# Performance work log

Measured on AMD Instinct MI355X. Metric: run time of the kernel, lower is better.

The kernel has to match this reference:

```python
import jax, jax.numpy as jnp
import numpy as np

B, T, I = 16384, 50, 5
H = 128
PRED_LEN = 12


def _uniform(key, shape, bound):
    return jax.random.uniform(key, shape, jnp.float32, -bound, bound)


def setup_inputs() -> dict:
    key = jax.random.key(0)
    ks = jax.random.split(key, 12)
    bound = 1.0 / np.sqrt(H)  # PyTorch LSTM/Linear default init
    return {
        "x": jax.random.normal(ks[0], (B, T, I), jnp.float32),
        "enc_Wih": _uniform(ks[1], (4 * H, I), bound),
        "enc_Whh": _uniform(ks[2], (4 * H, H), bound),
        "enc_bih": _uniform(ks[3], (4 * H,), bound),
        "enc_bhh": _uniform(ks[4], (4 * H,), bound),
        "dec_Wih": _uniform(ks[5], (4 * H, I), bound),
        "dec_Whh": _uniform(ks[6], (4 * H, H), bound),
        "dec_bih": _uniform(ks[7], (4 * H,), bound),
        "dec_bhh": _uniform(ks[8], (4 * H,), bound),
        "lin_W": _uniform(ks[9], (2, H), bound),
        "lin_b": _uniform(ks[10], (2,), bound),
    }


def _lstm_cell(x_t, h, c, Wih, Whh, bih, bhh):
    # PyTorch gate order: i, f, g, o
    gates = x_t @ Wih.T + h @ Whh.T + (bih + bhh)  # [B, 4H]
    i, f, g, o = jnp.split(gates, 4, axis=-1)
    i = jax.nn.sigmoid(i)
    f = jax.nn.sigmoid(f)
    g = jnp.tanh(g)
    o = jax.nn.sigmoid(o)
    c_new = f * c + i * g
    h_new = o * jnp.tanh(c_new)
    return h_new, c_new


def reference(x, enc_Wih, enc_Whh, enc_bih, enc_bhh,
              dec_Wih, dec_Whh, dec_bih, dec_bhh, lin_W, lin_b):
    b = x.shape[0]
    h0 = jnp.zeros((b, H), x.dtype)
    c0 = jnp.zeros((b, H), x.dtype)

    # ---- encoder LSTM over the history sequence ----
    def enc_step(carry, x_t):
        h, c = carry
        h, c = _lstm_cell(x_t, h, c, enc_Wih, enc_Whh, enc_bih, enc_bhh)
        return (h, c), None

    (h, c), _ = jax.lax.scan(enc_step, (h0, c0), jnp.swapaxes(x, 0, 1))

    static_context = x[:, -1, 2:]          # [B, I-2]
    last_velocity = x[:, -1, :2]           # [B, 2]
    dec_in0 = jnp.concatenate([last_velocity, static_context], axis=1)  # [B, I]

    def dec_step(carry, _):
        h, c, dec_in = carry
        h, c = _lstm_cell(dec_in, h, c, dec_Wih, dec_Whh, dec_bih, dec_bhh)
        pred = h @ lin_W.T + lin_b                      # [B, 2]
        dec_in = jnp.concatenate([pred, static_context], axis=1)
        return (h, c, dec_in), pred

    _, preds = jax.lax.scan(dec_step, (h, c, dec_in0), None, length=PRED_LEN)
    return jnp.swapaxes(preds, 0, 1)  # [B, pred_len, 2]
```

## Files before the change

### kernel.cpp

```cpp
#include <hip/hip_runtime.h>
#include <cstdint>

#define TT 50
#define II 5
#define PRED 12
#define SAMP 32
#define NSB 2

typedef _Float16 f16;
typedef _Float16 f16x8 __attribute__((ext_vector_type(8)));
typedef float f32x4 __attribute__((ext_vector_type(4)));

__device__ __forceinline__ float fsig(float x) {
    return __builtin_amdgcn_rcpf(1.f + __builtin_amdgcn_exp2f(-1.4426950408889634f * x));
}
__device__ __forceinline__ float ftanh(float x) {
    return 1.f - 2.f * __builtin_amdgcn_rcpf(1.f + __builtin_amdgcn_exp2f(2.885390081777927f * x));
}

__device__ __forceinline__ void mfma(f32x4& d, f16x8 a, f16x8 b) {
    asm("v_mfma_f32_16x16x32_f16 %0, %1, %2, %0" : "+v"(d) : "v"(a), "v"(b));
}

__device__ __forceinline__ void load_frags(const float* __restrict__ Wih,
                                           const float* __restrict__ Whh,
                                           const float* __restrict__ bih,
                                           const float* __restrict__ bhh,
                                           int w, int q, int cl, f16x8 wr[4][5]) {
    #pragma unroll
    for (int gs = 0; gs < 4; ++gs) {
        const int gw = gs * 128 + w * 16 + cl;
        const float* whr = Whh + gw * 128 + q * 8;
        #pragma unroll
        for (int kc = 0; kc < 4; ++kc) {
            f32x4 a = *(const f32x4*)(whr + kc * 32);
            f32x4 b = *(const f32x4*)(whr + kc * 32 + 4);
            f16x8 f;
            f[0] = (f16)a[0]; f[1] = (f16)a[1]; f[2] = (f16)a[2]; f[3] = (f16)a[3];
            f[4] = (f16)b[0]; f[5] = (f16)b[1]; f[6] = (f16)b[2]; f[7] = (f16)b[3];
            wr[gs][kc] = f;
        }
        f16x8 f;
        #pragma unroll
        for (int j = 0; j < 8; ++j) f[j] = (f16)0.f;
        if (q == 0) {
            f[0] = (f16)Wih[gw * 5 + 0]; f[1] = (f16)Wih[gw * 5 + 1];
            f[2] = (f16)Wih[gw * 5 + 2]; f[3] = (f16)Wih[gw * 5 + 3];
            f[4] = (f16)Wih[gw * 5 + 4];
            f[5] = (f16)(bih[gw] + bhh[gw]);
        }
        wr[gs][4] = f;
    }
}

__global__ __launch_bounds__(512, 2)
void lstm_kernel(const float* __restrict__ x,
                 const float* __restrict__ eWih, const float* __restrict__ eWhh,
                 const float* __restrict__ ebih, const float* __restrict__ ebhh,
                 const float* __restrict__ dWih, const float* __restrict__ dWhh,
                 const float* __restrict__ dbih, const float* __restrict__ dbhh,
                 const float* __restrict__ linW, const float* __restrict__ linB,
                 float* __restrict__ out) {
    __shared__ __align__(16) unsigned char state[2 * SAMP * 256];
    __shared__ __align__(16) f16 xstage[52 * SAMP * 8];
    __shared__ float predpart[8][SAMP][2];

    const int tid  = threadIdx.x;
    const int lane = tid & 63;
    const int w    = tid >> 6;
    const int q    = lane >> 4;
    const int cl   = lane & 15;
    const int s0   = blockIdx.x * SAMP;
    const int jb   = w * 16 + q * 4;
    const int fswz = (2 * (cl & 7)) | (cl >> 3);

    int hro[4];
    #pragma unroll
    for (int kc = 0; kc < 4; ++kc)
        hro[kc] = cl * 256 + (((kc * 4 + q) ^ fswz) & 15) * 16;
    const int physh = ((jb >> 3) ^ fswz) & 15;
    const int hwo   = cl * 256 + physh * 16 + (jb & 7) * 2;

    {
        uint32_t* sp = (uint32_t*)state;
        #pragma unroll
        for (int r = 0; r < 4; ++r) sp[tid + r * 512] = 0u;
    }
    #pragma unroll
    for (int k = 0; k < 4; ++k) {
        int c = tid + k * 512;
        if (c < TT * SAMP) {
            int t = c >> 5, s = c & 31;
            const float* xr = x + (size_t)(s0 + s) * (TT * II) + t * II;
            union { f16 h[8]; uint4 u; } pk;
            pk.h[0] = (f16)xr[0]; pk.h[1] = (f16)xr[1]; pk.h[2] = (f16)xr[2];
            pk.h[3] = (f16)xr[3]; pk.h[4] = (f16)xr[4];
            pk.h[5] = (f16)1.f;  pk.h[6] = (f16)0.f;  pk.h[7] = (f16)0.f;
            *(uint4*)(xstage + (t * SAMP + s) * 8) = pk.u;
        }
    }

    f16x8 wr[4][5];
    load_frags(eWih, eWhh, ebih, ebhh, w, q, cl, wr);

    float creg[NSB][4];
    #pragma unroll
    for (int ns = 0; ns < NSB; ++ns)
        #pragma unroll
        for (int i = 0; i < 4; ++i) creg[ns][i] = 0.f;

    __syncthreads();

    #pragma unroll 1
    for (int t = 0; t < TT; ++t) {
        const int curoff = (t & 1) << 13;
        const int nxtoff = curoff ^ 8192;
        #pragma unroll
        for (int ns = 0; ns < NSB; ++ns) {
            const unsigned char* cb = state + curoff + ns * 4096;
            f16x8 bx = *(const f16x8*)(xstage + (t * SAMP + ns * 16 + cl) * 8);
            f16x8 b0 = *(const f16x8*)(cb + hro[0]);
            f32x4 a0 = {0.f, 0.f, 0.f, 0.f};
            f32x4 a1 = {0.f, 0.f, 0.f, 0.f};
            f32x4 a2 = {0.f, 0.f, 0.f, 0.f};
            f32x4 a3 = {0.f, 0.f, 0.f, 0.f};
            mfma(a0, wr[0][0], b0);
            mfma(a1, wr[1][0], b0);
            mfma(a2, wr[2][0], b0);
            mfma(a3, wr[3][0], b0);
            #pragma unroll
            for (int kc = 1; kc < 4; ++kc) {
                f16x8 bh = *(const f16x8*)(cb + hro[kc]);
                mfma(a0, wr[0][kc], bh);
                mfma(a1, wr[1][kc], bh);
                mfma(a2, wr[2][kc], bh);
                mfma(a3, wr[3][kc], bh);
            }
            mfma(a0, wr[0][4], bx);
            mfma(a1, wr[1][4], bx);
            mfma(a2, wr[2][4], bx);
            mfma(a3, wr[3][4], bx);

            union { f16 h[4]; uint2 u; } pk;
            #pragma unroll
            for (int idx = 0; idx < 4; ++idx) {
                float ii = fsig(a0[idx]);
                float ff = fsig(a1[idx]);
                float gg = ftanh(a2[idx]);
                float oo = fsig(a3[idx]);
                float cn = ff * creg[ns][idx] + ii * gg;
                creg[ns][idx] = cn;
                pk.h[idx] = (f16)(oo * ftanh(cn));
            }
            *(uint2*)(state + nxtoff + ns * 4096 + hwo) = pk.u;
        }
        __syncthreads();
    }

    load_frags(dWih, dWhh, dbih, dbhh, w, q, cl, wr);
    f16 w0h[4], w1h[4];
    #pragma unroll
    for (int idx = 0; idx < 4; ++idx) {
        w0h[idx] = (f16)linW[jb + idx];
        w1h[idx] = (f16)linW[128 + jb + idx];
    }
    float sc0 = 0.f, sc1 = 0.f, sc2 = 0.f, lb0 = 0.f, lb1 = 0.f;
    if (tid < SAMP) {
        const float* xr = x + (size_t)(s0 + tid) * (TT * II) + 49 * II;
        sc0 = xr[2]; sc1 = xr[3]; sc2 = xr[4];
        lb0 = linB[0]; lb1 = linB[1];
    }

    #pragma unroll 1
    for (int td = 0; td < PRED; ++td) {
        const int curoff = (td & 1) << 13;
        const int nxtoff = curoff ^ 8192;
        const int xslot  = (td == 0) ? 49 : (50 + (td & 1));
        float p0s[NSB], p1s[NSB];
        #pragma unroll
        for (int ns = 0; ns < NSB; ++ns) {
            const unsigned char* cb = state + curoff + ns * 4096;
            f16x8 bx = *(const f16x8*)(xstage + (xslot * SAMP + ns * 16 + cl) * 8);
            f16x8 b0 = *(const f16x8*)(cb + hro[0]);
            f32x4 a0 = {0.f, 0.f, 0.f, 0.f};
            f32x4 a1 = {0.f, 0.f, 0.f, 0.f};
            f32x4 a2 = {0.f, 0.f, 0.f, 0.f};
            f32x4 a3 = {0.f, 0.f, 0.f, 0.f};
            mfma(a0, wr[0][0], b0);
            mfma(a1, wr[1][0], b0);
            mfma(a2, wr[2][0], b0);
            mfma(a3, wr[3][0], b0);
            #pragma unroll
            for (int kc = 1; kc < 4; ++kc) {
                f16x8 bh = *(const f16x8*)(cb + hro[kc]);
                mfma(a0, wr[0][kc], bh);
                mfma(a1, wr[1][kc], bh);
                mfma(a2, wr[2][kc], bh);
                mfma(a3, wr[3][kc], bh);
            }
            mfma(a0, wr[0][4], bx);
            mfma(a1, wr[1][4], bx);
            mfma(a2, wr[2][4], bx);
            mfma(a3, wr[3][4], bx);

            float p0 = 0.f, p1 = 0.f;
            union { f16 h[4]; uint2 u; } pk;
            #pragma unroll
            for (int idx = 0; idx < 4; ++idx) {
                float ii = fsig(a0[idx]);
                float ff = fsig(a1[idx]);
                float gg = ftanh(a2[idx]);
                float oo = fsig(a3[idx]);
                float cn = ff * creg[ns][idx] + ii * gg;
                creg[ns][idx] = cn;
                float hv = oo * ftanh(cn);
                p0 += hv * (float)w0h[idx];
                p1 += hv * (float)w1h[idx];
                pk.h[idx] = (f16)hv;
            }
            *(uint2*)(state + nxtoff + ns * 4096 + hwo) = pk.u;
            p0 += __shfl_xor(p0, 16); p0 += __shfl_xor(p0, 32);
            p1 += __shfl_xor(p1, 16); p1 += __shfl_xor(p1, 32);
            p0s[ns] = p0; p1s[ns] = p1;
        }
        if (q == 0) {
            #pragma unroll
            for (int ns = 0; ns < NSB; ++ns) {
                predpart[w][ns * 16 + cl][0] = p0s[ns];
                predpart[w][ns * 16 + cl][1] = p1s[ns];
            }
        }
        __syncthreads();
        if (tid < SAMP) {
            float a0 = lb0, a1 = lb1;
            #pragma unroll
            for (int ww = 0; ww < 8; ++ww) {
                a0 += predpart[ww][tid][0];
                a1 += predpart[ww][tid][1];
            }
            float2 o2; o2.x = a0; o2.y = a1;
            *(float2*)(out + (size_t)(s0 + tid) * (PRED * 2) + td * 2) = o2;
            union { f16 h[8]; uint4 u; } pk;
            pk.h[0] = (f16)a0;  pk.h[1] = (f16)a1;
            pk.h[2] = (f16)sc0; pk.h[3] = (f16)sc1; pk.h[4] = (f16)sc2;
            pk.h[5] = (f16)1.f; pk.h[6] = (f16)0.f; pk.h[7] = (f16)0.f;
            int ws = 50 + ((td + 1) & 1);
            *(uint4*)(xstage + (ws * SAMP + tid) * 8) = pk.u;
        }
        __syncthreads();
    }
}

extern "C" void kernel_launch(void* const* d_in, const int* in_sizes, int n_in,
                              void* d_out, int out_size, void* d_ws, size_t ws_size,
                              hipStream_t stream) {
    (void)in_sizes; (void)n_in; (void)out_size; (void)d_ws; (void)ws_size;
    const float* x    = (const float*)d_in[0];
    const float* eWih = (const float*)d_in[1];
    const float* eWhh = (const float*)d_in[2];
    const float* ebih = (const float*)d_in[3];
    const float* ebhh = (const float*)d_in[4];
    const float* dWih = (const float*)d_in[5];
    const float* dWhh = (const float*)d_in[6];
    const float* dbih = (const float*)d_in[7];
    const float* dbhh = (const float*)d_in[8];
    const float* linW = (const float*)d_in[9];
    const float* linB = (const float*)d_in[10];

    lstm_kernel<<<512, 512, 0, stream>>>(x, eWih, eWhh, ebih, ebhh,
                                         dWih, dWhh, dbih, dbhh,
                                         linW, linB, (float*)d_out);
}
```

Baseline: 311.2 us.

## Ping-pong two sample groups per block to overlap MFMA with gate math

Each block now handles 64 samples split into two independent 32-sample groups, each with its own hidden-state buffer and cell registers. The encoder and decoder loops alternate between the groups, issuing one group's matrix multiplies while the other group runs its sigmoid/tanh gate math. The intent is to hide the dependency between each step's MFMAs and the VALU work that follows them. The cost is half as many blocks (256), more live accumulator registers, larger LDS use, and more barriers per step in the decoder.

Result: faster. 284.7 us (-8.5%).

```diff
diff --git a/kernel.cpp b/kernel.cpp
--- a/kernel.cpp
+++ b/kernel.cpp
@@ -4,8 +4,6 @@
 #define TT 50
 #define II 5
 #define PRED 12
-#define SAMP 32
-#define NSB 2
 
 typedef _Float16 f16;
 typedef _Float16 f16x8 __attribute__((ext_vector_type(8)));
@@ -16,10 +14,6 @@
 }
 __device__ __forceinline__ float ftanh(float x) {
     return 1.f - 2.f * __builtin_amdgcn_rcpf(1.f + __builtin_amdgcn_exp2f(2.885390081777927f * x));
-}
-
-__device__ __forceinline__ void mfma(f32x4& d, f16x8 a, f16x8 b) {
-    asm("v_mfma_f32_16x16x32_f16 %0, %1, %2, %0" : "+v"(d) : "v"(a), "v"(b));
 }
 
 __device__ __forceinline__ void load_frags(const float* __restrict__ Wih,
@@ -50,6 +44,102 @@
             f[5] = (f16)(bih[gw] + bhh[gw]);
         }
         wr[gs][4] = f;
+    }
+}
+
+__device__ __forceinline__ void mfma_group(f32x4 (&acc)[4][2],
+        const unsigned char* hb, const f16* xrow,
+        const f16x8 (&wr)[4][5],
+        const int (&hro)[4], int cl) {
+    const f32x4 z4 = {0.f, 0.f, 0.f, 0.f};
+    #pragma unroll
+    for (int ns = 0; ns < 2; ++ns) {
+        const unsigned char* cb = hb + ns * 4096;
+        f16x8 bx = *(const f16x8*)(xrow + (ns * 16 + cl) * 8);
+        f16x8 b0 = *(const f16x8*)(cb + hro[0]);
+        acc[0][ns] = __builtin_amdgcn_mfma_f32_16x16x32_f16(wr[0][0], b0, z4, 0, 0, 0);
+        acc[1][ns] = __builtin_amdgcn_mfma_f32_16x16x32_f16(wr[1][0], b0, z4, 0, 0, 0);
+        acc[2][ns] = __builtin_amdgcn_mfma_f32_16x16x32_f16(wr[2][0], b0, z4, 0, 0, 0);
+        acc[3][ns] = __builtin_amdgcn_mfma_f32_16x16x32_f16(wr[3][0], b0, z4, 0, 0, 0);
+        #pragma unroll
+        for (int kc = 1; kc < 4; ++kc) {
+            f16x8 bh = *(const f16x8*)(cb + hro[kc]);
+            acc[0][ns] = __builtin_amdgcn_mfma_f32_16x16x32_f16(wr[0][kc], bh, acc[0][ns], 0, 0, 0);
+            acc[1][ns] = __builtin_amdgcn_mfma_f32_16x16x32_f16(wr[1][kc], bh, acc[1][ns], 0, 0, 0);
+            acc[2][ns] = __builtin_amdgcn_mfma_f32_16x16x32_f16(wr[2][kc], bh, acc[2][ns], 0, 0, 0);
+            acc[3][ns] = __builtin_amdgcn_mfma_f32_16x16x32_f16(wr[3][kc], bh, acc[3][ns], 0, 0, 0);
+        }
+        acc[0][ns] = __builtin_amdgcn_mfma_f32_16x16x32_f16(wr[0][4], bx, acc[0][ns], 0, 0, 0);
+        acc[1][ns] = __builtin_amdgcn_mfma_f32_16x16x32_f16(wr[1][4], bx, acc[1][ns], 0, 0, 0);
+        acc[2][ns] = __builtin_amdgcn_mfma_f32_16x16x32_f16(wr[2][4], bx, acc[2][ns], 0, 0, 0);
+        acc[3][ns] = __builtin_amdgcn_mfma_f32_16x16x32_f16(wr[3][4], bx, acc[3][ns], 0, 0, 0);
+    }
+}
+
+__device__ __forceinline__ void valu_enc(f32x4 (&acc)[4][2], float (&cr)[2][4],
+        unsigned char* hb, int hwo) {
+    #pragma unroll
+    for (int ns = 0; ns < 2; ++ns) {
+        union { f16 h[4]; uint2 u; } pk;
+        #pragma unroll
+        for (int idx = 0; idx < 4; ++idx) {
+            float ii = fsig(acc[0][ns][idx]);
+            float ff = fsig(acc[1][ns][idx]);
+            float gg = ftanh(acc[2][ns][idx]);
+            float oo = fsig(acc[3][ns][idx]);
+            float cn = ff * cr[ns][idx] + ii * gg;
+            cr[ns][idx] = cn;
+            pk.h[idx] = (f16)(oo * ftanh(cn));
+        }
+        *(uint2*)(hb + ns * 4096 + hwo) = pk.u;
+    }
+}
+
+__device__ __forceinline__ void valu_dec(f32x4 (&acc)[4][2], float (&cr)[2][4],
+        unsigned char* hb, int hwo,
+        const f16 (&w0h)[4], const f16 (&w1h)[4],
+        float (*pp)[32][2], int w, int q, int cl) {
+    #pragma unroll
+    for (int ns = 0; ns < 2; ++ns) {
+        union { f16 h[4]; uint2 u; } pk;
+        float p0 = 0.f, p1 = 0.f;
+        #pragma unroll
+        for (int idx = 0; idx < 4; ++idx) {
+            float ii = fsig(acc[0][ns][idx]);
+            float ff = fsig(acc[1][ns][idx]);
+            float gg = ftanh(acc[2][ns][idx]);
+            float oo = fsig(acc[3][ns][idx]);
+            float cn = ff * cr[ns][idx] + ii * gg;
+            cr[ns][idx] = cn;
+            float hv = oo * ftanh(cn);
+            p0 += hv * (float)w0h[idx];
+            p1 += hv * (float)w1h[idx];
+            pk.h[idx] = (f16)hv;
+        }
+        *(uint2*)(hb + ns * 4096 + hwo) = pk.u;
+        p0 += __shfl_xor(p0, 16); p0 += __shfl_xor(p0, 32);
+        p1 += __shfl_xor(p1, 16); p1 += __shfl_xor(p1, 32);
+        if (q == 0) { pp[w][ns * 16 + cl][0] = p0; pp[w][ns * 16 + cl][1] = p1; }
+    }
+}
+
+__device__ __forceinline__ void finalize(int g, int tdf, int tid, int s0,
+        const float (*pp)[32][2], float lb0, float lb1,
+        f16* xstage, float* __restrict__ out) {
+    if (tid < 32) {
+        float a0 = lb0, a1 = lb1;
+        #pragma unroll
+        for (int ww = 0; ww < 8; ++ww) { a0 += pp[ww][tid][0]; a1 += pp[ww][tid][1]; }
+        const int s = g * 32 + tid;
+        float2 o2; o2.x = a0; o2.y = a1;
+        *(float2*)(out + (size_t)(s0 + s) * (PRED * 2) + tdf * 2) = o2;
+        if (tdf < PRED - 1) {
+            uint4 row = *(const uint4*)(xstage + (49 * 64 + s) * 8);
+            union { f16 h[2]; uint32_t u; } pk2;
+            pk2.h[0] = (f16)a0; pk2.h[1] = (f16)a1;
+            row.x = pk2.u;
+            *(uint4*)(xstage + ((50 + g) * 64 + s) * 8) = row;
+        }
     }
 }
 
@@ -61,16 +151,16 @@
                  const float* __restrict__ dbih, const float* __restrict__ dbhh,
                  const float* __restrict__ linW, const float* __restrict__ linB,
                  float* __restrict__ out) {
-    __shared__ __align__(16) unsigned char state[2 * SAMP * 256];
-    __shared__ __align__(16) f16 xstage[52 * SAMP * 8];
-    __shared__ float predpart[8][SAMP][2];
+    __shared__ __align__(16) unsigned char hstate[2 * 8192];
+    __shared__ __align__(16) f16 xstage[52 * 64 * 8];
+    __shared__ float predpart[2][8][32][2];
 
     const int tid  = threadIdx.x;
     const int lane = tid & 63;
     const int w    = tid >> 6;
     const int q    = lane >> 4;
     const int cl   = lane & 15;
-    const int s0   = blockIdx.x * SAMP;
+    const int s0   = blockIdx.x * 64;
     const int jb   = w * 16 + q * 4;
     const int fswz = (2 * (cl & 7)) | (cl >> 3);
 
@@ -82,80 +172,55 @@
     const int hwo   = cl * 256 + physh * 16 + (jb & 7) * 2;
 
     {
-        uint32_t* sp = (uint32_t*)state;
-        #pragma unroll
-        for (int r = 0; r < 4; ++r) sp[tid + r * 512] = 0u;
-    }
-    #pragma unroll
-    for (int k = 0; k < 4; ++k) {
+        uint32_t* sp = (uint32_t*)hstate;
+        #pragma unroll
+        for (int r = 0; r < 8; ++r) sp[tid + r * 512] = 0u;
+    }
+    #pragma unroll
+    for (int k = 0; k < 7; ++k) {
         int c = tid + k * 512;
-        if (c < TT * SAMP) {
-            int t = c >> 5, s = c & 31;
+        if (c < TT * 64) {
+            int t = c >> 6, s = c & 63;
             const float* xr = x + (size_t)(s0 + s) * (TT * II) + t * II;
             union { f16 h[8]; uint4 u; } pk;
             pk.h[0] = (f16)xr[0]; pk.h[1] = (f16)xr[1]; pk.h[2] = (f16)xr[2];
             pk.h[3] = (f16)xr[3]; pk.h[4] = (f16)xr[4];
             pk.h[5] = (f16)1.f;  pk.h[6] = (f16)0.f;  pk.h[7] = (f16)0.f;
-            *(uint4*)(xstage + (t * SAMP + s) * 8) = pk.u;
+            *(uint4*)(xstage + (t * 64 + s) * 8) = pk.u;
         }
     }
 
     f16x8 wr[4][5];
     load_frags(eWih, eWhh, ebih, ebhh, w, q, cl, wr);
 
-    float creg[NSB][4];
-    #pragma unroll
-    for (int ns = 0; ns < NSB; ++ns)
-        #pragma unroll
-        for (int i = 0; i < 4; ++i) creg[ns][i] = 0.f;
-
-    __syncthreads();
-
+    float creg0[2][4], creg1[2][4];
+    #pragma unroll
+    for (int ns = 0; ns < 2; ++ns)
+        #pragma unroll
+        for (int i = 0; i < 4; ++i) { creg0[ns][i] = 0.f; creg1[ns][i] = 0.f; }
+
+    f32x4 accA[4][2], accB[4][2];
+    unsigned char* hb0 = hstate;
+    unsigned char* hb1 = hstate + 8192;
+
+    __syncthreads();
+
+    mfma_group(accA, hb0, xstage + 0, wr, hro, cl);
+    __syncthreads();
     #pragma unroll 1
-    for (int t = 0; t < TT; ++t) {
-        const int curoff = (t & 1) << 13;
-        const int nxtoff = curoff ^ 8192;
-        #pragma unroll
-        for (int ns = 0; ns < NSB; ++ns) {
-            const unsigned char* cb = state + curoff + ns * 4096;
-            f16x8 bx = *(const f16x8*)(xstage + (t * SAMP + ns * 16 + cl) * 8);
-            f16x8 b0 = *(const f16x8*)(cb + hro[0]);
-            f32x4 a0 = {0.f, 0.f, 0.f, 0.f};
-            f32x4 a1 = {0.f, 0.f, 0.f, 0.f};
-            f32x4 a2 = {0.f, 0.f, 0.f, 0.f};
-            f32x4 a3 = {0.f, 0.f, 0.f, 0.f};
-            mfma(a0, wr[0][0], b0);
-            mfma(a1, wr[1][0], b0);
-            mfma(a2, wr[2][0], b0);
-            mfma(a3, wr[3][0], b0);
-            #pragma unroll
-            for (int kc = 1; kc < 4; ++kc) {
-                f16x8 bh = *(const f16x8*)(cb + hro[kc]);
-                mfma(a0, wr[0][kc], bh);
-                mfma(a1, wr[1][kc], bh);
-                mfma(a2, wr[2][kc], bh);
-                mfma(a3, wr[3][kc], bh);
-            }
-            mfma(a0, wr[0][4], bx);
-            mfma(a1, wr[1][4], bx);
-            mfma(a2, wr[2][4], bx);
-            mfma(a3, wr[3][4], bx);
-
-            union { f16 h[4]; uint2 u; } pk;
-            #pragma unroll
-            for (int idx = 0; idx < 4; ++idx) {
-                float ii = fsig(a0[idx]);
-                float ff = fsig(a1[idx]);
-                float gg = ftanh(a2[idx]);
-                float oo = fsig(a3[idx]);
-                float cn = ff * creg[ns][idx] + ii * gg;
-                creg[ns][idx] = cn;
-                pk.h[idx] = (f16)(oo * ftanh(cn));
-            }
-            *(uint2*)(state + nxtoff + ns * 4096 + hwo) = pk.u;
-        }
-        __syncthreads();
-    }
+    for (int j = 0; j < 49; ++j) {
+        valu_enc(accA, creg0, hb0, hwo);
+        mfma_group(accB, hb1, xstage + (j * 64 + 32) * 8, wr, hro, cl);
+        __syncthreads();
+        valu_enc(accB, creg1, hb1, hwo);
+        mfma_group(accA, hb0, xstage + ((j + 1) * 64) * 8, wr, hro, cl);
+        __syncthreads();
+    }
+    valu_enc(accA, creg0, hb0, hwo);
+    mfma_group(accB, hb1, xstage + (49 * 64 + 32) * 8, wr, hro, cl);
+    __syncthreads();
+    valu_enc(accB, creg1, hb1, hwo);
+    __syncthreads();
 
     load_frags(dWih, dWhh, dbih, dbhh, w, q, cl, wr);
     f16 w0h[4], w1h[4];
@@ -164,91 +229,31 @@
         w0h[idx] = (f16)linW[jb + idx];
         w1h[idx] = (f16)linW[128 + jb + idx];
     }
-    float sc0 = 0.f, sc1 = 0.f, sc2 = 0.f, lb0 = 0.f, lb1 = 0.f;
-    if (tid < SAMP) {
-        const float* xr = x + (size_t)(s0 + tid) * (TT * II) + 49 * II;
-        sc0 = xr[2]; sc1 = xr[3]; sc2 = xr[4];
-        lb0 = linB[0]; lb1 = linB[1];
-    }
-
+    const float lb0 = linB[0], lb1 = linB[1];
+
+    mfma_group(accA, hb0, xstage + (49 * 64) * 8, wr, hro, cl);
+    __syncthreads();
+    valu_dec(accA, creg0, hb0, hwo, w0h, w1h, predpart[0], w, q, cl);
+    mfma_group(accB, hb1, xstage + (49 * 64 + 32) * 8, wr, hro, cl);
+    __syncthreads();
     #pragma unroll 1
-    for (int td = 0; td < PRED; ++td) {
-        const int curoff = (td & 1) << 13;
-        const int nxtoff = curoff ^ 8192;
-        const int xslot  = (td == 0) ? 49 : (50 + (td & 1));
-        float p0s[NSB], p1s[NSB];
-        #pragma unroll
-        for (int ns = 0; ns < NSB; ++ns) {
-            const unsigned char* cb = state + curoff + ns * 4096;
-            f16x8 bx = *(const f16x8*)(xstage + (xslot * SAMP + ns * 16 + cl) * 8);
-            f16x8 b0 = *(const f16x8*)(cb + hro[0]);
-            f32x4 a0 = {0.f, 0.f, 0.f, 0.f};
-            f32x4 a1 = {0.f, 0.f, 0.f, 0.f};
-            f32x4 a2 = {0.f, 0.f, 0.f, 0.f};
-            f32x4 a3 = {0.f, 0.f, 0.f, 0.f};
-            mfma(a0, wr[0][0], b0);
-            mfma(a1, wr[1][0], b0);
-            mfma(a2, wr[2][0], b0);
-            mfma(a3, wr[3][0], b0);
-            #pragma unroll
-            for (int kc = 1; kc < 4; ++kc) {
-                f16x8 bh = *(const f16x8*)(cb + hro[kc]);
-                mfma(a0, wr[0][kc], bh);
-                mfma(a1, wr[1][kc], bh);
-                mfma(a2, wr[2][kc], bh);
-                mfma(a3, wr[3][kc], bh);
-            }
-            mfma(a0, wr[0][4], bx);
-            mfma(a1, wr[1][4], bx);
-            mfma(a2, wr[2][4], bx);
-            mfma(a3, wr[3][4], bx);
-
-            float p0 = 0.f, p1 = 0.f;
-            union { f16 h[4]; uint2 u; } pk;
-            #pragma unroll
-            for (int idx = 0; idx < 4; ++idx) {
-                float ii = fsig(a0[idx]);
-                float ff = fsig(a1[idx]);
-                float gg = ftanh(a2[idx]);
-                float oo = fsig(a3[idx]);
-                float cn = ff * creg[ns][idx] + ii * gg;
-                creg[ns][idx] = cn;
-                float hv = oo * ftanh(cn);
-                p0 += hv * (float)w0h[idx];
-                p1 += hv * (float)w1h[idx];
-                pk.h[idx] = (f16)hv;
-            }
-            *(uint2*)(state + nxtoff + ns * 4096 + hwo) = pk.u;
-            p0 += __shfl_xor(p0, 16); p0 += __shfl_xor(p0, 32);
-            p1 += __shfl_xor(p1, 16); p1 += __shfl_xor(p1, 32);
-            p0s[ns] = p0; p1s[ns] = p1;
-        }
-        if (q == 0) {
-            #pragma unroll
-            for (int ns = 0; ns < NSB; ++ns) {
-                predpart[w][ns * 16 + cl][0] = p0s[ns];
-                predpart[w][ns * 16 + cl][1] = p1s[ns];
-            }
-        }
-        __syncthreads();
-        if (tid < SAMP) {
-            float a0 = lb0, a1 = lb1;
-            #pragma unroll
-            for (int ww = 0; ww < 8; ++ww) {
-                a0 += predpart[ww][tid][0];
-                a1 += predpart[ww][tid][1];
-            }
-            float2 o2; o2.x = a0; o2.y = a1;
-            *(float2*)(out + (size_t)(s0 + tid) * (PRED * 2) + td * 2) = o2;
-            union { f16 h[8]; uint4 u; } pk;
-            pk.h[0] = (f16)a0;  pk.h[1] = (f16)a1;
-            pk.h[2] = (f16)sc0; pk.h[3] = (f16)sc1; pk.h[4] = (f16)sc2;
-            pk.h[5] = (f16)1.f; pk.h[6] = (f16)0.f; pk.h[7] = (f16)0.f;
-            int ws = 50 + ((td + 1) & 1);
-            *(uint4*)(xstage + (ws * SAMP + tid) * 8) = pk.u;
-        }
-        __syncthreads();
-    }
+    for (int td = 1; td <= 11; ++td) {
+        finalize(0, td - 1, tid, s0, predpart[0], lb0, lb1, xstage, out);
+        __syncthreads();
+        valu_dec(accB, creg1, hb1, hwo, w0h, w1h, predpart[1], w, q, cl);
+        mfma_group(accA, hb0, xstage + (50 * 64) * 8, wr, hro, cl);
+        __syncthreads();
+        finalize(1, td - 1, tid, s0, predpart[1], lb0, lb1, xstage, out);
+        __syncthreads();
+        valu_dec(accA, creg0, hb0, hwo, w0h, w1h, predpart[0], w, q, cl);
+        mfma_group(accB, hb1, xstage + (51 * 64 + 32) * 8, wr, hro, cl);
+        __syncthreads();
+    }
+    finalize(0, 11, tid, s0, predpart[0], lb0, lb1, xstage, out);
+    __syncthreads();
+    valu_dec(accB, creg1, hb1, hwo, w0h, w1h, predpart[1], w, q, cl);
+    __syncthreads();
+    finalize(1, 11, tid, s0, predpart[1], lb0, lb1, xstage, out);
 }
 
 extern "C" void kernel_launch(void* const* d_in, const int* in_sizes, int n_in,
@@ -267,7 +272,7 @@
     const float* linW = (const float*)d_in[9];
     const float* linB = (const float*)d_in[10];
 
-    lstm_kernel<<<512, 512, 0, stream>>>(x, eWih, eWhh, ebih, ebhh,
+    lstm_kernel<<<256, 512, 0, stream>>>(x, eWih, eWhh, ebih, ebhh,
                                          dWih, dWhh, dbih, dbhh,
                                          linW, linB, (float*)d_out);
 }
```
